# Kernel tuning notes

Hardware: AMD Instinct MI355X
Metric: run time of the kernel (lower is better)

Reference implementation:

```python
import jax, jax.numpy as jnp
import numpy as np

NEG_INF = -9e15
ALPHA = 2.0  # LeakyReLU negative slope from init (alpha=2)


def setup_inputs() -> dict:
    key = jax.random.key(0)
    k1, k2, k3, k4 = jax.random.split(key, 4)
    B, N, Fin, Fout = 8, 2048, 256, 128
    x = jax.random.normal(k1, (B, N, Fin), dtype=jnp.float32)
    adj = jax.random.randint(k2, (B, N, N), 0, 2, dtype=jnp.int32)
    # xavier_uniform with gain=1.414
    def xavier(k, shape, gain=1.414):
        fan_in, fan_out = shape[0], shape[1]
        bound = gain * np.sqrt(6.0 / (fan_in + fan_out))
        return jax.random.uniform(k, shape, jnp.float32, -bound, bound)
    W = xavier(k3, (Fin, Fout))
    a = xavier(k4, (2 * Fout, 1))
    return {"x": x, "adj": adj, "W": W, "a": a}


def reference(x, adj, W, a):
    # Wh: [B, N, Fout]
    Wh = jnp.matmul(x, W)
    Fout = W.shape[1]
    a1 = a[:Fout, 0]   # [Fout]
    a2 = a[Fout:, 0]   # [Fout]
    f1 = jnp.einsum('bnf,f->bn', Wh, a1)  # [B, N]
    f2 = jnp.einsum('bnf,f->bn', Wh, a2)  # [B, N]
    e = f1[:, :, None] + f2[:, None, :]   # [B, N, N]
    e = jnp.where(e >= 0, e, ALPHA * e)   # leaky relu, slope 2
    e = jnp.where(adj > 0, e, NEG_INF)
    attention = jax.nn.softmax(e, axis=2)
    # dropout: eval mode (no-op)
    h_prime = jnp.matmul(attention, Wh)   # [B, N, Fout]
    # concat=True -> elu
    return jnp.where(h_prime > 0, h_prime, jnp.expm1(h_prime))
```

## Files before the change

### kernel.cpp

```cpp
#include <hip/hip_runtime.h>
#include <hip/hip_bf16.h>
#include <math.h>

constexpr int B_   = 8;
constexpr int N_   = 2048;
constexpr int FIN  = 256;
constexpr int FOUT = 128;

constexpr int CH  = 512;
constexpr int NCH = N_ / CH;
constexpr int PR  = CH + 8;
constexpr int XR  = FIN + 8;
constexpr int TR  = 40;

typedef __attribute__((ext_vector_type(8))) short bf16x8;
typedef __attribute__((ext_vector_type(4))) float f32x4;
typedef __attribute__((ext_vector_type(4))) int   i32x4;

static __device__ __forceinline__ unsigned short f2bf(float f) {
    __hip_bfloat16 h = __float2bfloat16(f);
    return *reinterpret_cast<unsigned short*>(&h);
}
static __device__ __forceinline__ i32x4 ntload4(const int* p) {
    return __builtin_nontemporal_load((const i32x4*)p);
}

__global__ __launch_bounds__(256) void k0_wt(const float* __restrict__ W,
                                             unsigned short* __restrict__ Wt) {
    const int n = blockIdx.x;
    const int k = threadIdx.x;
    Wt[n * FIN + k] = f2bf(W[k * FOUT + n]);
}

__global__ __launch_bounds__(256) void ka_wh(const float* __restrict__ x,
                                             const unsigned short* __restrict__ Wt,
                                             const float* __restrict__ a,
                                             unsigned short* __restrict__ WhT,
                                             float* __restrict__ f1,
                                             float* __restrict__ f2) {
    __shared__ unsigned short xs[32 * XR];
    __shared__ float as[2 * FOUT];
    __shared__ float fred[2][4][32];

    const int tid = threadIdx.x;
    const int j0  = blockIdx.x * 32;
    const int b   = j0 >> 11;
    const int jb  = j0 & (N_ - 1);

    if (tid < 2 * FOUT) as[tid] = a[tid];
    {
        const float4* xsrc = (const float4*)(x + (size_t)j0 * FIN);
#pragma unroll
        for (int t = 0; t < 8; ++t) {
            const int idx = tid + t * 256;
            float4 v = xsrc[idx];
            const int row = idx >> 6, c4 = idx & 63;
            ushort4 u;
            u.x = f2bf(v.x); u.y = f2bf(v.y); u.z = f2bf(v.z); u.w = f2bf(v.w);
            *(ushort4*)&xs[row * XR + c4 * 4] = u;
        }
    }
    __syncthreads();

    const int wave = tid >> 6, lane = tid & 63;
    const int quad = lane >> 4, l16 = lane & 15;

    f32x4 acc[2][2];
#pragma unroll
    for (int aa = 0; aa < 2; ++aa)
#pragma unroll
        for (int nn = 0; nn < 2; ++nn) acc[aa][nn] = {0.f, 0.f, 0.f, 0.f};

    const unsigned short* wtA0 = Wt + (size_t)(32 * wave + l16) * FIN;
    const unsigned short* wtA1 = wtA0 + 16 * FIN;
#pragma unroll
    for (int ks = 0; ks < FIN / 32; ++ks) {
        const int kof = ks * 32 + quad * 8;
        bf16x8 af0 = *(const bf16x8*)&wtA0[kof];
        bf16x8 af1 = *(const bf16x8*)&wtA1[kof];
        bf16x8 bf0 = *(const bf16x8*)&xs[l16 * XR + kof];
        bf16x8 bf1 = *(const bf16x8*)&xs[(16 + l16) * XR + kof];
        acc[0][0] = __builtin_amdgcn_mfma_f32_16x16x32_bf16(af0, bf0, acc[0][0], 0, 0, 0);
        acc[0][1] = __builtin_amdgcn_mfma_f32_16x16x32_bf16(af0, bf1, acc[0][1], 0, 0, 0);
        acc[1][0] = __builtin_amdgcn_mfma_f32_16x16x32_bf16(af1, bf0, acc[1][0], 0, 0, 0);
        acc[1][1] = __builtin_amdgcn_mfma_f32_16x16x32_bf16(af1, bf1, acc[1][1], 0, 0, 0);
    }
    __syncthreads();

    unsigned short* T = xs;
    float pf[2][2] = {{0.f, 0.f}, {0.f, 0.f}};
#pragma unroll
    for (int aa = 0; aa < 2; ++aa)
#pragma unroll
        for (int nn = 0; nn < 2; ++nn)
#pragma unroll
            for (int r = 0; r < 4; ++r) {
                const int d = 32 * wave + 16 * aa + 4 * quad + r;
                const float v = acc[aa][nn][r];
                T[d * TR + nn * 16 + l16] = f2bf(v);
                pf[0][nn] += v * as[d];
                pf[1][nn] += v * as[FOUT + d];
            }
#pragma unroll
    for (int ff = 0; ff < 2; ++ff)
#pragma unroll
        for (int nn = 0; nn < 2; ++nn) {
            float v = pf[ff][nn];
            v += __shfl_xor(v, 16);
            v += __shfl_xor(v, 32);
            pf[ff][nn] = v;
        }
    if (quad == 0) {
#pragma unroll
        for (int ff = 0; ff < 2; ++ff)
#pragma unroll
            for (int nn = 0; nn < 2; ++nn)
                fred[ff][wave][nn * 16 + l16] = pf[ff][nn];
    }
    __syncthreads();

    unsigned short* dstW = WhT + (size_t)b * FOUT * N_;
#pragma unroll
    for (int it = 0; it < 2; ++it) {
        const int idx = it * 256 + tid;
        const int d = idx >> 2, q = idx & 3;
        bf16x8 v = *(const bf16x8*)&T[d * TR + q * 8];
        *(bf16x8*)&dstW[(size_t)d * N_ + jb + q * 8] = v;
    }
    if (tid < 64) {
        const int ff = tid >> 5, j32 = tid & 31;
        const float s = fred[ff][0][j32] + fred[ff][1][j32] +
                        fred[ff][2][j32] + fred[ff][3][j32];
        (ff ? f2 : f1)[(size_t)b * N_ + jb + j32] = s;
    }
}

static __device__ __forceinline__ void kb_phaseA(
    const int c, const int lane, const int pw, const int i0,
    const int* __restrict__ adjB, const float4* __restrict__ f2b4,
    const float* __restrict__ f1r, float* __restrict__ s_run,
    unsigned short* __restrict__ pb)
{
    const float4 fv0 = f2b4[c * (CH / 4) + lane];
    const float4 fv1 = f2b4[c * (CH / 4) + 64 + lane];
#pragma unroll
    for (int rr = 0; rr < 4; ++rr) {
        const int ti = pw * 4 + rr;
        const int i  = i0 + ti;
        const int* arow = adjB + (size_t)i * N_ + c * CH;
        const i32x4 av0 = ntload4(arow + 4 * lane);
        const i32x4 av1 = ntload4(arow + 256 + 4 * lane);
        const float f1i = f1r[rr];

        float e[8];
        e[0] = f1i + fv0.x; e[1] = f1i + fv0.y; e[2] = f1i + fv0.z; e[3] = f1i + fv0.w;
        e[4] = f1i + fv1.x; e[5] = f1i + fv1.y; e[6] = f1i + fv1.z; e[7] = f1i + fv1.w;
#pragma unroll
        for (int q = 0; q < 8; ++q) e[q] = (e[q] >= 0.f) ? e[q] : 2.f * e[q];

        float pv[8];
        pv[0] = (av0.x > 0) ? __expf(e[0]) : 0.f;
        pv[1] = (av0.y > 0) ? __expf(e[1]) : 0.f;
        pv[2] = (av0.z > 0) ? __expf(e[2]) : 0.f;
        pv[3] = (av0.w > 0) ? __expf(e[3]) : 0.f;
        pv[4] = (av1.x > 0) ? __expf(e[4]) : 0.f;
        pv[5] = (av1.y > 0) ? __expf(e[5]) : 0.f;
        pv[6] = (av1.z > 0) ? __expf(e[6]) : 0.f;
        pv[7] = (av1.w > 0) ? __expf(e[7]) : 0.f;
        s_run[rr] += ((pv[0] + pv[1]) + (pv[2] + pv[3])) +
                     ((pv[4] + pv[5]) + (pv[6] + pv[7]));

        ushort4 u0, u1;
        u0.x = f2bf(pv[0]); u0.y = f2bf(pv[1]); u0.z = f2bf(pv[2]); u0.w = f2bf(pv[3]);
        u1.x = f2bf(pv[4]); u1.y = f2bf(pv[5]); u1.z = f2bf(pv[6]); u1.w = f2bf(pv[7]);
        *(ushort4*)&pb[ti * PR + 4 * lane]       = u0;
        *(ushort4*)&pb[ti * PR + 256 + 4 * lane] = u1;
    }
}

__global__ __launch_bounds__(512, 8) void kb_attn(const int* __restrict__ adj,
                                                  const unsigned short* __restrict__ WhT,
                                                  const float* __restrict__ f1,
                                                  const float* __restrict__ f2,
                                                  float* __restrict__ out) {
    __shared__ unsigned short p[2][16 * PR];
    __shared__ float rs[16];

    const int tid  = threadIdx.x;
    const int b    = blockIdx.x & 7;
    const int i0   = (blockIdx.x >> 3) * 16;
    const int wave = tid >> 6, lane = tid & 63;
    const int quad = lane >> 4, l16 = lane & 15;
    const bool producer = (wave < 4);
    const int  pw = wave & 3;

    const float4* f2b4 = (const float4*)(f2 + (size_t)b * N_);
    const int*    adjB = adj + (size_t)b * N_ * N_;

    float f1r[4], s_run[4];
#pragma unroll
    for (int rr = 0; rr < 4; ++rr) {
        f1r[rr]   = f1[(size_t)b * N_ + i0 + pw * 4 + rr];
        s_run[rr] = 0.f;
    }

    f32x4 acc0 = {0.f, 0.f, 0.f, 0.f}, acc1 = {0.f, 0.f, 0.f, 0.f};
    const int n0 = pw * 32;
    const unsigned short* wB0 = WhT + (size_t)b * FOUT * N_ + (size_t)(n0 + l16) * N_;
    const unsigned short* wB1 = wB0 + (size_t)16 * N_;

    for (int step = 0; step <= NCH; ++step) {
        if (producer) {
            if (step < NCH) {
                kb_phaseA(step, lane, pw, i0, adjB, f2b4, f1r, s_run,
                          &p[step & 1][0]);
            } else {
#pragma unroll
                for (int rr = 0; rr < 4; ++rr) {
                    float s = s_run[rr];
#pragma unroll
                    for (int o = 32; o; o >>= 1) s += __shfl_xor(s, o);
                    if (lane == 0) rs[pw * 4 + rr] = s;
                }
            }
        } else if (step >= 1) {
            const int c = step - 1;
            const unsigned short* pA = &p[c & 1][l16 * PR];
            const int kbase = c * CH;
#pragma unroll
            for (int ks = 0; ks < CH / 32; ++ks) {
                const int kof = ks * 32 + quad * 8;
                bf16x8 afr = *(const bf16x8*)&pA[kof];
                bf16x8 b0  = *(const bf16x8*)&wB0[kbase + kof];
                bf16x8 b1  = *(const bf16x8*)&wB1[kbase + kof];
                acc0 = __builtin_amdgcn_mfma_f32_16x16x32_bf16(afr, b0, acc0, 0, 0, 0);
                acc1 = __builtin_amdgcn_mfma_f32_16x16x32_bf16(afr, b1, acc1, 0, 0, 0);
            }
        }
        __syncthreads();
    }

    if (!producer) {
#pragma unroll
        for (int r = 0; r < 4; ++r) {
            const int m = quad * 4 + r;
            const float inv = 1.f / rs[m];
            float v0 = acc0[r] * inv;
            float v1 = acc1[r] * inv;
            v0 = (v0 > 0.f) ? v0 : expm1f(v0);
            v1 = (v1 > 0.f) ? v1 : expm1f(v1);
            const size_t base = ((size_t)b * N_ + i0 + m) * FOUT + n0;
            out[base + l16]      = v0;
            out[base + 16 + l16] = v1;
        }
    }
}

extern "C" void kernel_launch(void* const* d_in, const int* in_sizes, int n_in,
                              void* d_out, int out_size, void* d_ws, size_t ws_size,
                              hipStream_t stream) {
    const float* x   = (const float*)d_in[0];
    const int*   adj = (const int*)d_in[1];
    const float* W   = (const float*)d_in[2];
    const float* a   = (const float*)d_in[3];
    float* out = (float*)d_out;

    unsigned short* WhT = (unsigned short*)d_ws;
    unsigned short* Wt  = WhT + (size_t)B_ * FOUT * N_;
    float* f1 = (float*)(Wt + (size_t)FOUT * FIN);
    float* f2 = f1 + (size_t)B_ * N_;

    hipLaunchKernelGGL(k0_wt, dim3(FOUT), dim3(FIN), 0, stream, W, Wt);
    hipLaunchKernelGGL(ka_wh, dim3(B_ * N_ / 32), dim3(256), 0, stream,
                       x, Wt, a, WhT, f1, f2);
    hipLaunchKernelGGL(kb_attn, dim3(B_ * N_ / 16), dim3(512), 0, stream,
                       adj, WhT, f1, f2, out);
}
```

Measured before the change: 268.2 us.

## Pre-pack adjacency into bitmask in Wh kernel, read bits in attention

The Wh projection kernel gains extra blocks that read the int32 adjacency matrix and pack it into a 64-bit-per-64-columns bitmask using wave ballots. The attention kernel then reads 32-bit mask words and extracts per-lane 4-bit nibbles instead of streaming 16 bytes of int32 adjacency per lane per row. This moves the large adjacency read out of the MFMA/softmax kernel into a pure bandwidth pass, so the attention kernel's memory traffic shrinks substantially. The cost is an extra small mask write and read, the adjacency still being read once in full, and more workspace being used.

```diff
diff --git a/kernel.cpp b/kernel.cpp
--- a/kernel.cpp
+++ b/kernel.cpp
@@ -15,14 +15,10 @@
 
 typedef __attribute__((ext_vector_type(8))) short bf16x8;
 typedef __attribute__((ext_vector_type(4))) float f32x4;
-typedef __attribute__((ext_vector_type(4))) int   i32x4;
 
 static __device__ __forceinline__ unsigned short f2bf(float f) {
     __hip_bfloat16 h = __float2bfloat16(f);
     return *reinterpret_cast<unsigned short*>(&h);
-}
-static __device__ __forceinline__ i32x4 ntload4(const int* p) {
-    return __builtin_nontemporal_load((const i32x4*)p);
 }
 
 __global__ __launch_bounds__(256) void k0_wt(const float* __restrict__ W,
@@ -32,17 +28,39 @@
     Wt[n * FIN + k] = f2bf(W[k * FOUT + n]);
 }
 
-__global__ __launch_bounds__(256) void ka_wh(const float* __restrict__ x,
-                                             const unsigned short* __restrict__ Wt,
-                                             const float* __restrict__ a,
-                                             unsigned short* __restrict__ WhT,
-                                             float* __restrict__ f1,
-                                             float* __restrict__ f2) {
+__global__ __launch_bounds__(256) void kaj(const float* __restrict__ x,
+                                           const unsigned short* __restrict__ Wt,
+                                           const float* __restrict__ a,
+                                           const int* __restrict__ adj,
+                                           unsigned short* __restrict__ WhT,
+                                           float* __restrict__ f1,
+                                           float* __restrict__ f2,
+                                           unsigned long long* __restrict__ mask) {
     __shared__ unsigned short xs[32 * XR];
     __shared__ float as[2 * FOUT];
     __shared__ float fred[2][4][32];
 
     const int tid = threadIdx.x;
+
+    if (blockIdx.x >= 512) {
+        const int wave = tid >> 6, lane = tid & 63;
+        const size_t row = (size_t)(blockIdx.x - 512) * 4 + wave;
+        const int* src = adj + row * N_;
+        unsigned long long* dst = mask + row * (N_ / 64);
+#pragma unroll
+        for (int g = 0; g < 4; ++g) {
+            unsigned long long m[8];
+#pragma unroll
+            for (int q = 0; q < 8; ++q)
+                m[q] = __ballot(src[g * 512 + q * 64 + lane] > 0);
+            unsigned long long v = m[0];
+#pragma unroll
+            for (int q = 1; q < 8; ++q) v = (lane == q) ? m[q] : v;
+            if (lane < 8) dst[g * 8 + lane] = v;
+        }
+        return;
+    }
+
     const int j0  = blockIdx.x * 32;
     const int b   = j0 >> 11;
     const int jb  = j0 & (N_ - 1);
@@ -137,7 +155,7 @@
 
 static __device__ __forceinline__ void kb_phaseA(
     const int c, const int lane, const int pw, const int i0,
-    const int* __restrict__ adjB, const float4* __restrict__ f2b4,
+    const unsigned int* __restrict__ maskB, const float4* __restrict__ f2b4,
     const float* __restrict__ f1r, float* __restrict__ s_run,
     unsigned short* __restrict__ pb)
 {
@@ -147,9 +165,11 @@
     for (int rr = 0; rr < 4; ++rr) {
         const int ti = pw * 4 + rr;
         const int i  = i0 + ti;
-        const int* arow = adjB + (size_t)i * N_ + c * CH;
-        const i32x4 av0 = ntload4(arow + 4 * lane);
-        const i32x4 av1 = ntload4(arow + 256 + 4 * lane);
+        const unsigned int* mrow = maskB + (size_t)i * (N_ / 32);
+        const unsigned int w0 = mrow[c * 16 + (lane >> 3)];
+        const unsigned int w1 = mrow[c * 16 + 8 + (lane >> 3)];
+        const unsigned int t0 = (w0 >> ((lane & 7) * 4)) & 0xF;
+        const unsigned int t1 = (w1 >> ((lane & 7) * 4)) & 0xF;
         const float f1i = f1r[rr];
 
         float e[8];
@@ -159,14 +179,14 @@
         for (int q = 0; q < 8; ++q) e[q] = (e[q] >= 0.f) ? e[q] : 2.f * e[q];
 
         float pv[8];
-        pv[0] = (av0.x > 0) ? __expf(e[0]) : 0.f;
-        pv[1] = (av0.y > 0) ? __expf(e[1]) : 0.f;
-        pv[2] = (av0.z > 0) ? __expf(e[2]) : 0.f;
-        pv[3] = (av0.w > 0) ? __expf(e[3]) : 0.f;
-        pv[4] = (av1.x > 0) ? __expf(e[4]) : 0.f;
-        pv[5] = (av1.y > 0) ? __expf(e[5]) : 0.f;
-        pv[6] = (av1.z > 0) ? __expf(e[6]) : 0.f;
-        pv[7] = (av1.w > 0) ? __expf(e[7]) : 0.f;
+        pv[0] = (t0 & 1u) ? __expf(e[0]) : 0.f;
+        pv[1] = (t0 & 2u) ? __expf(e[1]) : 0.f;
+        pv[2] = (t0 & 4u) ? __expf(e[2]) : 0.f;
+        pv[3] = (t0 & 8u) ? __expf(e[3]) : 0.f;
+        pv[4] = (t1 & 1u) ? __expf(e[4]) : 0.f;
+        pv[5] = (t1 & 2u) ? __expf(e[5]) : 0.f;
+        pv[6] = (t1 & 4u) ? __expf(e[6]) : 0.f;
+        pv[7] = (t1 & 8u) ? __expf(e[7]) : 0.f;
         s_run[rr] += ((pv[0] + pv[1]) + (pv[2] + pv[3])) +
                      ((pv[4] + pv[5]) + (pv[6] + pv[7]));
 
@@ -178,7 +198,7 @@
     }
 }
 
-__global__ __launch_bounds__(512, 8) void kb_attn(const int* __restrict__ adj,
+__global__ __launch_bounds__(512, 8) void kb_attn(const unsigned int* __restrict__ mask32,
                                                   const unsigned short* __restrict__ WhT,
                                                   const float* __restrict__ f1,
                                                   const float* __restrict__ f2,
@@ -195,7 +215,7 @@
     const int  pw = wave & 3;
 
     const float4* f2b4 = (const float4*)(f2 + (size_t)b * N_);
-    const int*    adjB = adj + (size_t)b * N_ * N_;
+    const unsigned int* maskB = mask32 + (size_t)b * N_ * (N_ / 32);
 
     float f1r[4], s_run[4];
 #pragma unroll
@@ -212,7 +232,7 @@
     for (int step = 0; step <= NCH; ++step) {
         if (producer) {
             if (step < NCH) {
-                kb_phaseA(step, lane, pw, i0, adjB, f2b4, f1r, s_run,
+                kb_phaseA(step, lane, pw, i0, maskB, f2b4, f1r, s_run,
                           &p[step & 1][0]);
             } else {
 #pragma unroll
@@ -269,10 +289,11 @@
     unsigned short* Wt  = WhT + (size_t)B_ * FOUT * N_;
     float* f1 = (float*)(Wt + (size_t)FOUT * FIN);
     float* f2 = f1 + (size_t)B_ * N_;
+    unsigned long long* mask = (unsigned long long*)(f2 + (size_t)B_ * N_);
 
     hipLaunchKernelGGL(k0_wt, dim3(FOUT), dim3(FIN), 0, stream, W, Wt);
-    hipLaunchKernelGGL(ka_wh, dim3(B_ * N_ / 32), dim3(256), 0, stream,
-                       x, Wt, a, WhT, f1, f2);
+    hipLaunchKernelGGL(kaj, dim3(512 + B_ * N_ / 4), dim3(256), 0, stream,
+                       x, Wt, a, adj, WhT, f1, f2, mask);
     hipLaunchKernelGGL(kb_attn, dim3(B_ * N_ / 16), dim3(512), 0, stream,
-                       adj, WhT, f1, f2, out);
-}
+                       (const unsigned int*)mask, WhT, f1, f2, out);
+}
```

Result: slower. 275.6 us (+2.8%).
